# Optimization experiments

Hardware: AMD Instinct MI355X
Metric: run time of the kernel (lower is better)

Reference implementation:

```python
import jax, jax.numpy as jnp
import numpy as np

K, B, N, V = 16, 512, 4096, 32  # concepts, test batch, train points, concept cardinality
EPS = 1e-13


def setup_inputs() -> dict:
    key = jax.random.key(0)
    k1, k2, k3 = jax.random.split(key, 3)
    c_p = jax.random.normal(k1, (K, B, V), dtype=jnp.float32)          # concept logits per test sample
    c_in = jax.random.randint(k2, (N, K), 0, V, dtype=jnp.int32)        # train concept labels
    delta_in = jax.random.randint(k3, (N,), 0, 2).astype(jnp.float32)   # censoring indicators
    bandwidth = jnp.ones((1,), dtype=jnp.float32)
    return {"c_in": c_in, "delta_in": delta_in, "c_p": c_p, "bandwidth": bandwidth}


def _forward(c_in, delta_in, c_p, bandwidth):
    # ---- SimpleGauss kernel weights ----
    p = jax.nn.softmax(c_p, axis=-1)                       # [K, B, V]
    sum_sq = jnp.sum(p * p, axis=-1)                       # [K, B]
    # scatter_reduce(-1 at label) then sum of squares == sum(p^2) - 2*p[label] + 1
    idx = jnp.broadcast_to(c_in.T[:, None, :], (K, B, N))  # [K, B, N]
    gathered = jnp.take_along_axis(p, idx, axis=-1)        # [K, B, N]
    metric = jnp.sum(sum_sq[:, :, None] - 2.0 * gathered + 1.0, axis=0)  # [B, N]
    bw = jnp.clip(bandwidth, 0.1, 10.0)                    # [1]
    w = jnp.exp(-metric / bw)                              # [B, N]
    s = jnp.sum(w, axis=1, keepdims=True)                  # sum over train points (dim=-2 of [B,N,1])
    bad = s < EPS
    W = jnp.where(bad, 0.0, w / jnp.where(bad, 1.0, s))    # [B, N]

    # ---- Beran estimator chain ----
    w_cumsum = jnp.cumsum(W, axis=1)
    shifted = w_cumsum - W
    bad_idx = jnp.isclose(shifted, 1.0) | jnp.isclose(w_cumsum, 1.0)
    shifted = jnp.where(bad_idx, 0.0, shifted)
    wc = jnp.where(bad_idx, 0.0, w_cumsum)
    xi = jnp.log(1.0 - shifted) - jnp.log(1.0 - wc)        # [B, N]
    hazards = jnp.cumsum(delta_in[None, :] * xi, axis=1)
    surv_func = jnp.exp(-hazards)                          # [B, N]
    first_step = 1.0 - surv_func[:, :1]
    surv_steps = jnp.concatenate([first_step, surv_func[:, :-1] - surv_func[:, 1:]], axis=-1)
    s2 = jnp.sum(surv_steps, axis=-1, keepdims=True)
    bad2 = s2 < EPS
    surv_steps = jnp.where(bad2, 0.0, surv_steps / jnp.where(bad2, 1.0, s2))
    return surv_func, surv_steps


def reference(c_in, delta_in, c_p, bandwidth):
    return _forward(c_in, delta_in, c_p, bandwidth)
```

## Files before the change

### kernel.cpp

```cpp
#include <hip/hip_runtime.h>
#include <math.h>

#define K_ 16
#define B_ 512
#define N_ 4096
#define V_ 32
#define TPB 256
#define CH (N_ / TPB)
#define EPS_ 1e-13f

__global__ __launch_bounds__(TPB) void beran_kernel(
    const int* __restrict__ c_in, const float* __restrict__ delta_in,
    const float* __restrict__ c_p, const float* __restrict__ bandwidth,
    float* __restrict__ out) {
  __shared__ float p2[K_][V_];
  __shared__ float wbuf[N_];
  __shared__ float sumsq[K_];
  __shared__ float wscan[TPB / 64];
  __shared__ float s_base;

  const int b = blockIdx.x;
  const int t = threadIdx.x;
  const int lane = t & 63;
  const int wid = t >> 6;

  {
    const int k = t >> 4;
    const int sub = t & 15;
    const int v0 = sub * 2;
    const float* cp = c_p + ((size_t)k * B_ + b) * V_;
    float x0 = cp[v0], x1 = cp[v0 + 1];
    float m = fmaxf(x0, x1);
#pragma unroll
    for (int d = 1; d < 16; d <<= 1) m = fmaxf(m, __shfl_xor(m, d, 64));
    float e0 = expf(x0 - m), e1 = expf(x1 - m);
    float sum = e0 + e1;
#pragma unroll
    for (int d = 1; d < 16; d <<= 1) sum += __shfl_xor(sum, d, 64);
    float inv = 1.0f / sum;
    float p0 = e0 * inv, p1 = e1 * inv;
    p2[k][v0] = 2.0f * p0;
    p2[k][v0 + 1] = 2.0f * p1;
    float ss = p0 * p0 + p1 * p1;
#pragma unroll
    for (int d = 1; d < 16; d <<= 1) ss += __shfl_xor(ss, d, 64);
    if (sub == 0) sumsq[k] = ss;
  }
  __syncthreads();
  if (t == 0) {
    float bs = 0.f;
#pragma unroll
    for (int k = 0; k < K_; k++) bs += sumsq[k];
    s_base = bs + (float)K_;
  }
  __syncthreads();
  const float base = s_base;
  float bw = bandwidth[0];
  bw = fminf(fmaxf(bw, 0.1f), 10.0f);
  const float invbw = 1.0f / bw;

  const int4* crow = (const int4*)c_in;
  for (int n = t; n < N_; n += TPB) {
    int4 a = crow[n * 4 + 0];
    int4 bb = crow[n * 4 + 1];
    int4 cc = crow[n * 4 + 2];
    int4 dd = crow[n * 4 + 3];
    float g = p2[0][a.x] + p2[1][a.y] + p2[2][a.z] + p2[3][a.w]
            + p2[4][bb.x] + p2[5][bb.y] + p2[6][bb.z] + p2[7][bb.w]
            + p2[8][cc.x] + p2[9][cc.y] + p2[10][cc.z] + p2[11][cc.w]
            + p2[12][dd.x] + p2[13][dd.y] + p2[14][dd.z] + p2[15][dd.w];
    wbuf[n] = expf(-(base - g) * invbw);
  }
  __syncthreads();

  const int start = t * CH;
  float lv[CH];
  float tot = 0.f;
#pragma unroll
  for (int i = 0; i < CH; i++) { lv[i] = wbuf[start + i]; tot += lv[i]; }
  float inc = tot;
#pragma unroll
  for (int d = 1; d < 64; d <<= 1) {
    float u = __shfl_up(inc, d, 64);
    if (lane >= d) inc += u;
  }
  if (lane == 63) wscan[wid] = inc;
  __syncthreads();
  float s = 0.f, woff = 0.f;
#pragma unroll
  for (int j = 0; j < TPB / 64; j++) {
    float v = wscan[j];
    s += v;
    if (j < wid) woff += v;
  }
  const float inv_s = (s < EPS_) ? 0.f : 1.0f / s;
  float rawp = woff + (inc - tot);

  const float4* dl4 = (const float4*)delta_in;
  float dl[CH];
#pragma unroll
  for (int j = 0; j < CH / 4; j++) {
    float4 d4 = dl4[t * (CH / 4) + j];
    dl[j * 4 + 0] = d4.x; dl[j * 4 + 1] = d4.y;
    dl[j * 4 + 2] = d4.z; dl[j * 4 + 3] = d4.w;
  }
  const float thr = 1.001e-5f;
#pragma unroll
  for (int i = 0; i < CH; i++) {
    float sh = rawp * inv_s;
    rawp += lv[i];
    float wc = rawp * inv_s;
    float y = 0.f;
    bool bad = (fabsf(sh - 1.f) <= thr) || (fabsf(wc - 1.f) <= thr);
    if (dl[i] != 0.f && !bad)
      y = dl[i] * (logf(1.f - sh) - logf(1.f - wc));
    lv[i] = y;
  }
  __syncthreads();

  float tot2 = 0.f;
#pragma unroll
  for (int i = 0; i < CH; i++) tot2 += lv[i];
  float inc2 = tot2;
#pragma unroll
  for (int d = 1; d < 64; d <<= 1) {
    float u = __shfl_up(inc2, d, 64);
    if (lane >= d) inc2 += u;
  }
  if (lane == 63) wscan[wid] = inc2;
  __syncthreads();
  float hoff = 0.f;
#pragma unroll
  for (int j = 0; j < TPB / 64; j++) if (j < wid) hoff += wscan[j];
  float h = hoff + (inc2 - tot2);
#pragma unroll
  for (int i = 0; i < CH; i++) {
    h += lv[i];
    wbuf[start + i] = expf(-h);
  }
  __syncthreads();

  const float s2 = 1.0f - wbuf[N_ - 1];
  const float inv2 = (s2 < EPS_) ? 0.f : 1.0f / s2;
  float* out_s = out + (size_t)b * N_;
  float* out_t = out + (size_t)B_ * N_ + (size_t)b * N_;
  for (int n = t; n < N_; n += TPB) {
    float sv = wbuf[n];
    float pv = (n == 0) ? 1.0f : wbuf[n - 1];
    out_s[n] = sv;
    out_t[n] = (pv - sv) * inv2;
  }
}

extern "C" void kernel_launch(void* const* d_in, const int* in_sizes, int n_in,
                              void* d_out, int out_size, void* d_ws, size_t ws_size,
                              hipStream_t stream) {
  const int* c_in = (const int*)d_in[0];
  const float* delta_in = (const float*)d_in[1];
  const float* c_p = (const float*)d_in[2];
  const float* bandwidth = (const float*)d_in[3];
  float* outp = (float*)d_out;
  hipLaunchKernelGGL(beran_kernel, dim3(B_), dim3(TPB), 0, stream,
                     c_in, delta_in, c_p, bandwidth, outp);
}
```

Before: 77.72 us.

## Double block size, compute weights directly into registers, use fast exp/log intrinsics

Raises threads per block from 256 to 512, halving elements per thread to 8. The softmax now maps one value per thread. The weight computation writes straight into per-thread registers over a contiguous chunk, removing a shared-memory round trip and one barrier. expf and logf are replaced with the __expf and __logf intrinsics. In exchange, c_in reads become strided per thread (each thread reads 8 consecutive 64-byte rows), which may hurt coalescing, and the fast intrinsics lower accuracy in the log-difference hazard terms.

```diff
diff --git a/kernel.cpp b/kernel.cpp
--- a/kernel.cpp
+++ b/kernel.cpp
@@ -5,8 +5,9 @@
 #define B_ 512
 #define N_ 4096
 #define V_ 32
-#define TPB 256
+#define TPB 512
 #define CH (N_ / TPB)
+#define NW (TPB / 64)
 #define EPS_ 1e-13f
 
 __global__ __launch_bounds__(TPB) void beran_kernel(
@@ -16,7 +17,7 @@
   __shared__ float p2[K_][V_];
   __shared__ float wbuf[N_];
   __shared__ float sumsq[K_];
-  __shared__ float wscan[TPB / 64];
+  __shared__ float wscan[NW];
   __shared__ float s_base;
 
   const int b = blockIdx.x;
@@ -25,26 +26,22 @@
   const int wid = t >> 6;
 
   {
-    const int k = t >> 4;
-    const int sub = t & 15;
-    const int v0 = sub * 2;
-    const float* cp = c_p + ((size_t)k * B_ + b) * V_;
-    float x0 = cp[v0], x1 = cp[v0 + 1];
-    float m = fmaxf(x0, x1);
+    const int k = t >> 5;
+    const int v = t & 31;
+    float x = c_p[((size_t)k * B_ + b) * V_ + v];
+    float m = x;
 #pragma unroll
-    for (int d = 1; d < 16; d <<= 1) m = fmaxf(m, __shfl_xor(m, d, 64));
-    float e0 = expf(x0 - m), e1 = expf(x1 - m);
-    float sum = e0 + e1;
+    for (int d = 1; d < 32; d <<= 1) m = fmaxf(m, __shfl_xor(m, d, 64));
+    float e = __expf(x - m);
+    float sum = e;
 #pragma unroll
-    for (int d = 1; d < 16; d <<= 1) sum += __shfl_xor(sum, d, 64);
-    float inv = 1.0f / sum;
-    float p0 = e0 * inv, p1 = e1 * inv;
-    p2[k][v0] = 2.0f * p0;
-    p2[k][v0 + 1] = 2.0f * p1;
-    float ss = p0 * p0 + p1 * p1;
+    for (int d = 1; d < 32; d <<= 1) sum += __shfl_xor(sum, d, 64);
+    float p = e * (1.0f / sum);
+    p2[k][v] = 2.0f * p;
+    float ss = p * p;
 #pragma unroll
-    for (int d = 1; d < 16; d <<= 1) ss += __shfl_xor(ss, d, 64);
-    if (sub == 0) sumsq[k] = ss;
+    for (int d = 1; d < 32; d <<= 1) ss += __shfl_xor(ss, d, 64);
+    if (v == 0) sumsq[k] = ss;
   }
   __syncthreads();
   if (t == 0) {
@@ -59,8 +56,13 @@
   bw = fminf(fmaxf(bw, 0.1f), 10.0f);
   const float invbw = 1.0f / bw;
 
+  const int start = t * CH;
   const int4* crow = (const int4*)c_in;
-  for (int n = t; n < N_; n += TPB) {
+  float lv[CH];
+  float tot = 0.f;
+#pragma unroll
+  for (int i = 0; i < CH; i++) {
+    const int n = start + i;
     int4 a = crow[n * 4 + 0];
     int4 bb = crow[n * 4 + 1];
     int4 cc = crow[n * 4 + 2];
@@ -69,15 +71,10 @@
             + p2[4][bb.x] + p2[5][bb.y] + p2[6][bb.z] + p2[7][bb.w]
             + p2[8][cc.x] + p2[9][cc.y] + p2[10][cc.z] + p2[11][cc.w]
             + p2[12][dd.x] + p2[13][dd.y] + p2[14][dd.z] + p2[15][dd.w];
-    wbuf[n] = expf(-(base - g) * invbw);
+    float w = __expf(-(base - g) * invbw);
+    lv[i] = w;
+    tot += w;
   }
-  __syncthreads();
-
-  const int start = t * CH;
-  float lv[CH];
-  float tot = 0.f;
-#pragma unroll
-  for (int i = 0; i < CH; i++) { lv[i] = wbuf[start + i]; tot += lv[i]; }
   float inc = tot;
 #pragma unroll
   for (int d = 1; d < 64; d <<= 1) {
@@ -88,7 +85,7 @@
   __syncthreads();
   float s = 0.f, woff = 0.f;
 #pragma unroll
-  for (int j = 0; j < TPB / 64; j++) {
+  for (int j = 0; j < NW; j++) {
     float v = wscan[j];
     s += v;
     if (j < wid) woff += v;
@@ -113,7 +110,7 @@
     float y = 0.f;
     bool bad = (fabsf(sh - 1.f) <= thr) || (fabsf(wc - 1.f) <= thr);
     if (dl[i] != 0.f && !bad)
-      y = dl[i] * (logf(1.f - sh) - logf(1.f - wc));
+      y = dl[i] * (__logf(1.f - sh) - __logf(1.f - wc));
     lv[i] = y;
   }
   __syncthreads();
@@ -131,12 +128,12 @@
   __syncthreads();
   float hoff = 0.f;
 #pragma unroll
-  for (int j = 0; j < TPB / 64; j++) if (j < wid) hoff += wscan[j];
+  for (int j = 0; j < NW; j++) if (j < wid) hoff += wscan[j];
   float h = hoff + (inc2 - tot2);
 #pragma unroll
   for (int i = 0; i < CH; i++) {
     h += lv[i];
-    wbuf[start + i] = expf(-h);
+    wbuf[start + i] = __expf(-h);
   }
   __syncthreads();
 
```

Result: slower. 83.87 us (+7.9%).
